# Kernel optimization log

Measured on AMD Instinct MI355X. Metric: run time of the kernel, lower is better.

## Reference

```python
import jax, jax.numpy as jnp
import numpy as np

L, C, S = 4096, 128, 64
SAMPLE_RATE = 4096.0  # Hz; dt offset is 1/sample_rate as in the flax module


def setup_inputs() -> dict:
    key = jax.random.key(0)
    ks = jax.random.split(key, 4)
    x = jax.random.normal(ks[0], (L, C), dtype=jnp.float32)
    # S4D-real init: A = -arange(1, S+1), param stores log(-A) broadcast to (C, S)
    A_log = jnp.broadcast_to(
        jnp.log(jnp.arange(1, S + 1, dtype=jnp.float32)), (C, S)
    )
    sc = 1.0 / np.sqrt(C)  # lecun_normal-like scale for Dense kernels
    B_kernel = (jax.random.normal(ks[1], (C, S)) * sc).astype(jnp.float32)
    B_bias = jnp.zeros((S,), jnp.float32)
    C_kernel = (jax.random.normal(ks[2], (C, S)) * sc).astype(jnp.float32)
    C_bias = jnp.zeros((S,), jnp.float32)
    dt_kernel = (jax.random.normal(ks[3], (C, C)) * sc).astype(jnp.float32)
    dt_bias = jnp.zeros((C,), jnp.float32)
    return {
        "x": x,
        "A_log": A_log,
        "B_kernel": B_kernel,
        "B_bias": B_bias,
        "C_kernel": C_kernel,
        "C_bias": C_bias,
        "dt_kernel": dt_kernel,
        "dt_bias": dt_bias,
    }


def reference(x, A_log, B_kernel, B_bias, C_kernel, C_bias, dt_kernel, dt_bias):
    # ssm params
    A = -jnp.exp(A_log)                                   # (C, S), negative real
    B = 1.0 + x @ B_kernel + B_bias                       # (L, S)
    Cm = x @ C_kernel + C_bias                            # (L, S)
    dt = jax.nn.softplus(1.0 / SAMPLE_RATE + x @ dt_kernel + dt_bias)  # (L, C)
    # discretization (ZOH for diagonal real A)
    At = jnp.exp(A[None, :, :] * dt[:, :, None])          # (L, C, S)
    ut = (At - 1.0) * (B[:, None, :] / A[None, :, :]) * x[:, :, None]  # (L, C, S)

    # parallel linear-recurrence scan: h_t = At_t * h_{t-1} + ut_t, h0 = 0
    def comb(e1, e2):
        a1, u1 = e1
        a2, u2 = e2
        return (a2 * a1, a2 * u1 + u2)

    _, ht = jax.lax.associative_scan(comb, (At, ut))      # scans over axis 0 (L)
    y = jnp.einsum("ls,lcs->lc", Cm, ht)                  # (L, C)
    return y
```

## Files before the change

### kernel.cpp

```cpp
#include <hip/hip_runtime.h>
#include <math.h>

#define LL 4096
#define CC 128
#define SS 64
#define CLEN 32
#define GW 8
#define NG 16
#define CS 8192
#define LOG2E 1.44269504088896f

__global__ __launch_bounds__(256) void k_proj(
    const float* __restrict__ x,
    const float* __restrict__ Bk, const float* __restrict__ Bb,
    const float* __restrict__ Ck, const float* __restrict__ Cb,
    const float* __restrict__ Dk, const float* __restrict__ Db,
    float* __restrict__ Bmat, float* __restrict__ Cmat,
    float* __restrict__ DTmT, float* __restrict__ xT)
{
    __shared__ float xs[CC][20];
    const int r0 = blockIdx.x * 16;
    const int t = threadIdx.x;
    {
        const int r = t >> 4, k8 = (t & 15) * 8;
        const float4 v0 = *(const float4*)&x[(r0 + r) * CC + k8];
        const float4 v1 = *(const float4*)&x[(r0 + r) * CC + k8 + 4];
        xs[k8+0][r] = v0.x; xs[k8+1][r] = v0.y; xs[k8+2][r] = v0.z; xs[k8+3][r] = v0.w;
        xs[k8+4][r] = v1.x; xs[k8+5][r] = v1.y; xs[k8+6][r] = v1.z; xs[k8+7][r] = v1.w;
    }
    __syncthreads();
    {
        const int k = t >> 1, half = (t & 1) * 8;
        const float4 a = *(const float4*)&xs[k][half];
        const float4 b = *(const float4*)&xs[k][half + 4];
        *(float4*)&xT[k * LL + r0 + half]     = a;
        *(float4*)&xT[k * LL + r0 + half + 4] = b;
    }
    const int tc = t & 63, tr = t >> 6;
    const float* Wb; int wstride, wo;
    if (tc < 16)      { Wb = Bk; wstride = SS; wo = 4 * tc; }
    else if (tc < 32) { Wb = Ck; wstride = SS; wo = 4 * tc - 64; }
    else              { Wb = Dk; wstride = CC; wo = 4 * tc - 128; }
    float acc[4][4];
#pragma unroll
    for (int r = 0; r < 4; ++r)
#pragma unroll
        for (int j = 0; j < 4; ++j) acc[r][j] = 0.0f;
    for (int k = 0; k < CC; ++k) {
        const float4 wq = *(const float4*)(Wb + k * wstride + wo);
        const float4 xq = *(const float4*)&xs[k][4 * tr];
        const float wv[4] = {wq.x, wq.y, wq.z, wq.w};
        const float xv[4] = {xq.x, xq.y, xq.z, xq.w};
#pragma unroll
        for (int r = 0; r < 4; ++r)
#pragma unroll
            for (int j = 0; j < 4; ++j) acc[r][j] = fmaf(xv[r], wv[j], acc[r][j]);
    }
    const int rb = r0 + 4 * tr;
    if (tc < 32) {
        const float* bb = (tc < 16) ? Bb : Cb;
        const float add = (tc < 16) ? 1.0f : 0.0f;
        float bias[4];
#pragma unroll
        for (int j = 0; j < 4; ++j) bias[j] = add + bb[wo + j];
        float* dst = (tc < 16) ? Bmat : Cmat;
#pragma unroll
        for (int r = 0; r < 4; ++r) {
            const float4 o = make_float4(acc[r][0] + bias[0], acc[r][1] + bias[1],
                                         acc[r][2] + bias[2], acc[r][3] + bias[3]);
            *(float4*)&dst[(rb + r) * SS + wo] = o;
        }
    } else {
#pragma unroll
        for (int j = 0; j < 4; ++j) {
            const float bj = Db[wo + j] + 0.000244140625f;
            float sp[4];
#pragma unroll
            for (int r = 0; r < 4; ++r) {
                const float z = acc[r][j] + bj;
                sp[r] = fmaxf(z, 0.0f) + log1pf(__expf(-fabsf(z)));
            }
            *(float4*)&DTmT[(wo + j) * LL + rb] = make_float4(sp[0], sp[1], sp[2], sp[3]);
        }
    }
}

__global__ __launch_bounds__(512, 4) void k_sweep1(
    const float* __restrict__ xT, const float* __restrict__ A_log,
    const float* __restrict__ Bmat, const float* __restrict__ DTmT,
    float2* __restrict__ GaGu)
{
    __shared__ float2 agg[GW][SS];
    const int lane = threadIdx.x & 63;
    const int w = __builtin_amdgcn_readfirstlane(threadIdx.x >> 6);
    const int c = blockIdx.x >> 4;
    const int g = blockIdx.x & (NG - 1);
    const int j = c * SS + lane;
    const float A = -__expf(A_log[j]);
    const float A2 = A * LOG2E;
    const float invA = 1.0f / A;
    const int l0 = (g * GW + w) * CLEN;
    const float* dtp = DTmT + c * LL + l0;
    const float* xp  = xT   + c * LL + l0;
    const float* Bp  = Bmat + l0 * SS + lane;
    float ap = 1.0f, uc = 0.0f;
#pragma unroll
    for (int i = 0; i < CLEN; ++i) {
        const float At = __builtin_amdgcn_exp2f(A2 * dtp[i]);
        const float u  = (At - 1.0f) * invA * (Bp[i * SS] * xp[i]);
        ap *= At;
        uc = fmaf(At, uc, u);
    }
    agg[w][lane] = make_float2(ap, uc);
    __syncthreads();
    if (w == 0) {
        float ga = 1.0f, gu = 0.0f;
#pragma unroll
        for (int k = 0; k < GW; ++k) {
            const float2 t = agg[k][lane];
            gu = fmaf(t.x, gu, t.y);
            ga *= t.x;
        }
        GaGu[g * CS + j] = make_float2(ga, gu);
    }
}

__global__ __launch_bounds__(512) void k_emit(
    const float* __restrict__ xT, const float* __restrict__ A_log,
    const float* __restrict__ Bmat, const float* __restrict__ Cmat,
    const float* __restrict__ DTmT,
    const float2* __restrict__ GaGu,
    float* __restrict__ y)
{
    __shared__ float2 agg[GW][SS];
    __shared__ float hgs[SS];
    const int lane = threadIdx.x & 63;
    const int w = __builtin_amdgcn_readfirstlane(threadIdx.x >> 6);
    const int c = blockIdx.x >> 4;
    const int g = blockIdx.x & (NG - 1);
    const int j = c * SS + lane;
    const float A = -__expf(A_log[j]);
    const float A2 = A * LOG2E;
    const float invA = 1.0f / A;
    if (w == 0) {
        float hg = 0.0f;
        float2 ggr[NG - 1];
#pragma unroll
        for (int gg = 0; gg < NG - 1; ++gg) ggr[gg] = GaGu[gg * CS + j];
#pragma unroll
        for (int gg = 0; gg < NG - 1; ++gg)
            hg = (gg < g) ? fmaf(ggr[gg].x, hg, ggr[gg].y) : hg;
        hgs[lane] = hg;
    }
    const int l0 = (g * GW + w) * CLEN;
    const float* dtp = DTmT + c * LL + l0;
    const float* xp  = xT   + c * LL + l0;
    const float* Bp  = Bmat + l0 * SS + lane;
    const float* Cp  = Cmat + l0 * SS + lane;
    float at[CLEN], uu[CLEN];
    {
        float ap = 1.0f, uc = 0.0f;
#pragma unroll
        for (int i = 0; i < CLEN; ++i) {
            at[i] = __builtin_amdgcn_exp2f(A2 * dtp[i]);
            uu[i] = (at[i] - 1.0f) * invA * (Bp[i * SS] * xp[i]);
            ap *= at[i];
            uc = fmaf(at[i], uc, uu[i]);
        }
        agg[w][lane] = make_float2(ap, uc);
    }
    __syncthreads();
    const float hg = hgs[lane];
    float ea = 1.0f, eu = 0.0f;
    for (int k = 0; k < w; ++k) {
        const float2 t = agg[k][lane];
        eu = fmaf(t.x, eu, t.y);
        ea *= t.x;
    }
    float h = fmaf(ea, hg, eu);
#pragma unroll
    for (int i = 0; i < CLEN; ++i) {
        h = fmaf(at[i], h, uu[i]);
        uu[i] = Cp[i * SS] * h;
    }
#pragma unroll
    for (int k = 0; k < 5; ++k) {
        const int d = 1 << k;
        const bool hi = (lane & d) != 0;
#pragma unroll
        for (int i2 = 0; i2 < (CLEN >> (k + 1)); ++i2) {
            const float a = uu[2 * i2], b = uu[2 * i2 + 1];
            const float send = hi ? a : b;
            const float t = __shfl_xor(send, d, 64);
            uu[i2] = (hi ? b : a) + t;
        }
    }
    const float t = __shfl_xor(uu[0], 32, 64);
    const float yv = uu[0] + t;
    if (lane < 32) y[(l0 + lane) * CC + c] = yv;
}

extern "C" void kernel_launch(void* const* d_in, const int* in_sizes, int n_in,
                              void* d_out, int out_size, void* d_ws, size_t ws_size,
                              hipStream_t stream)
{
    const float* x  = (const float*)d_in[0];
    const float* Al = (const float*)d_in[1];
    const float* Bk = (const float*)d_in[2];
    const float* Bb = (const float*)d_in[3];
    const float* Ck = (const float*)d_in[4];
    const float* Cb = (const float*)d_in[5];
    const float* Dk = (const float*)d_in[6];
    const float* Db = (const float*)d_in[7];
    float* y  = (float*)d_out;
    float* ws = (float*)d_ws;

    float*  Bmat = ws;
    float*  Cmat = Bmat + LL * SS;
    float*  DTmT = Cmat + LL * SS;
    float*  xT   = DTmT + CC * LL;
    float2* GaGu = (float2*)(xT + CC * LL);

    k_proj  <<<LL / 16, 256, 0, stream>>>(x, Bk, Bb, Ck, Cb, Dk, Db, Bmat, Cmat, DTmT, xT);
    k_sweep1<<<CC * NG, 512, 0, stream>>>(xT, Al, Bmat, DTmT, GaGu);
    k_emit  <<<CC * NG, 512, 0, stream>>>(xT, Al, Bmat, Cmat, DTmT, GaGu, y);
}
```

Measured before the change: 46.92 us.

## Drop transposed x/dt buffers; stage per-channel dt and x columns in LDS

The projection kernel no longer writes a transposed copy of x, and it stores dt row-major instead of channel-major. The sweep and emit kernels now gather each block's 256 dt and x values for their channel into shared memory with strided loads, then read them from LDS inside the recurrence loop. This removes the transpose writes and their extra global traffic, and replaces the per-lane wave-uniform scalar global loads of dt and x. In exchange, the gather is strided by 128 floats (poorly coalesced), and each block adds an extra barrier before compute.

```diff
diff --git a/kernel.cpp b/kernel.cpp
--- a/kernel.cpp
+++ b/kernel.cpp
@@ -7,6 +7,7 @@
 #define CLEN 32
 #define GW 8
 #define NG 16
+#define GL 256
 #define CS 8192
 #define LOG2E 1.44269504088896f
 
@@ -15,8 +16,7 @@
     const float* __restrict__ Bk, const float* __restrict__ Bb,
     const float* __restrict__ Ck, const float* __restrict__ Cb,
     const float* __restrict__ Dk, const float* __restrict__ Db,
-    float* __restrict__ Bmat, float* __restrict__ Cmat,
-    float* __restrict__ DTmT, float* __restrict__ xT)
+    float* __restrict__ Bmat, float* __restrict__ Cmat, float* __restrict__ DTm)
 {
     __shared__ float xs[CC][20];
     const int r0 = blockIdx.x * 16;
@@ -29,13 +29,6 @@
         xs[k8+4][r] = v1.x; xs[k8+5][r] = v1.y; xs[k8+6][r] = v1.z; xs[k8+7][r] = v1.w;
     }
     __syncthreads();
-    {
-        const int k = t >> 1, half = (t & 1) * 8;
-        const float4 a = *(const float4*)&xs[k][half];
-        const float4 b = *(const float4*)&xs[k][half + 4];
-        *(float4*)&xT[k * LL + r0 + half]     = a;
-        *(float4*)&xT[k * LL + r0 + half + 4] = b;
-    }
     const int tc = t & 63, tr = t >> 6;
     const float* Wb; int wstride, wo;
     if (tc < 16)      { Wb = Bk; wstride = SS; wo = 4 * tc; }
@@ -71,43 +64,50 @@
             *(float4*)&dst[(rb + r) * SS + wo] = o;
         }
     } else {
-#pragma unroll
-        for (int j = 0; j < 4; ++j) {
-            const float bj = Db[wo + j] + 0.000244140625f;
+        float bias[4];
+#pragma unroll
+        for (int j = 0; j < 4; ++j) bias[j] = Db[wo + j] + 0.000244140625f;
+#pragma unroll
+        for (int r = 0; r < 4; ++r) {
             float sp[4];
 #pragma unroll
-            for (int r = 0; r < 4; ++r) {
-                const float z = acc[r][j] + bj;
-                sp[r] = fmaxf(z, 0.0f) + log1pf(__expf(-fabsf(z)));
+            for (int j = 0; j < 4; ++j) {
+                const float z = acc[r][j] + bias[j];
+                sp[j] = fmaxf(z, 0.0f) + log1pf(__expf(-fabsf(z)));
             }
-            *(float4*)&DTmT[(wo + j) * LL + rb] = make_float4(sp[0], sp[1], sp[2], sp[3]);
+            *(float4*)&DTm[(rb + r) * CC + wo] = make_float4(sp[0], sp[1], sp[2], sp[3]);
         }
     }
 }
 
 __global__ __launch_bounds__(512, 4) void k_sweep1(
-    const float* __restrict__ xT, const float* __restrict__ A_log,
-    const float* __restrict__ Bmat, const float* __restrict__ DTmT,
+    const float* __restrict__ x, const float* __restrict__ A_log,
+    const float* __restrict__ Bmat, const float* __restrict__ DTm,
     float2* __restrict__ GaGu)
 {
     __shared__ float2 agg[GW][SS];
-    const int lane = threadIdx.x & 63;
-    const int w = __builtin_amdgcn_readfirstlane(threadIdx.x >> 6);
+    __shared__ float dts[GL];
+    __shared__ float xss[GL];
+    const int t = threadIdx.x;
+    const int lane = t & 63;
+    const int w = __builtin_amdgcn_readfirstlane(t >> 6);
     const int c = blockIdx.x >> 4;
     const int g = blockIdx.x & (NG - 1);
+    const int gl0 = g * GL;
+    if (t < GL) dts[t]      = DTm[(gl0 + t) * CC + c];
+    else        xss[t - GL] = x[(gl0 + (t - GL)) * CC + c];
+    __syncthreads();
     const int j = c * SS + lane;
     const float A = -__expf(A_log[j]);
     const float A2 = A * LOG2E;
     const float invA = 1.0f / A;
-    const int l0 = (g * GW + w) * CLEN;
-    const float* dtp = DTmT + c * LL + l0;
-    const float* xp  = xT   + c * LL + l0;
-    const float* Bp  = Bmat + l0 * SS + lane;
+    const int lw = w * CLEN;
+    const float* Bp = Bmat + (gl0 + lw) * SS + lane;
     float ap = 1.0f, uc = 0.0f;
 #pragma unroll
     for (int i = 0; i < CLEN; ++i) {
-        const float At = __builtin_amdgcn_exp2f(A2 * dtp[i]);
-        const float u  = (At - 1.0f) * invA * (Bp[i * SS] * xp[i]);
+        const float At = __builtin_amdgcn_exp2f(A2 * dts[lw + i]);
+        const float u  = (At - 1.0f) * invA * (Bp[i * SS] * xss[lw + i]);
         ap *= At;
         uc = fmaf(At, uc, u);
     }
@@ -117,27 +117,33 @@
         float ga = 1.0f, gu = 0.0f;
 #pragma unroll
         for (int k = 0; k < GW; ++k) {
-            const float2 t = agg[k][lane];
-            gu = fmaf(t.x, gu, t.y);
-            ga *= t.x;
+            const float2 tt = agg[k][lane];
+            gu = fmaf(tt.x, gu, tt.y);
+            ga *= tt.x;
         }
         GaGu[g * CS + j] = make_float2(ga, gu);
     }
 }
 
 __global__ __launch_bounds__(512) void k_emit(
-    const float* __restrict__ xT, const float* __restrict__ A_log,
+    const float* __restrict__ x, const float* __restrict__ A_log,
     const float* __restrict__ Bmat, const float* __restrict__ Cmat,
-    const float* __restrict__ DTmT,
+    const float* __restrict__ DTm,
     const float2* __restrict__ GaGu,
     float* __restrict__ y)
 {
     __shared__ float2 agg[GW][SS];
     __shared__ float hgs[SS];
-    const int lane = threadIdx.x & 63;
-    const int w = __builtin_amdgcn_readfirstlane(threadIdx.x >> 6);
+    __shared__ float dts[GL];
+    __shared__ float xss[GL];
+    const int t = threadIdx.x;
+    const int lane = t & 63;
+    const int w = __builtin_amdgcn_readfirstlane(t >> 6);
     const int c = blockIdx.x >> 4;
     const int g = blockIdx.x & (NG - 1);
+    const int gl0 = g * GL;
+    if (t < GL) dts[t]      = DTm[(gl0 + t) * CC + c];
+    else        xss[t - GL] = x[(gl0 + (t - GL)) * CC + c];
     const int j = c * SS + lane;
     const float A = -__expf(A_log[j]);
     const float A2 = A * LOG2E;
@@ -152,18 +158,17 @@
             hg = (gg < g) ? fmaf(ggr[gg].x, hg, ggr[gg].y) : hg;
         hgs[lane] = hg;
     }
-    const int l0 = (g * GW + w) * CLEN;
-    const float* dtp = DTmT + c * LL + l0;
-    const float* xp  = xT   + c * LL + l0;
-    const float* Bp  = Bmat + l0 * SS + lane;
-    const float* Cp  = Cmat + l0 * SS + lane;
+    __syncthreads();
+    const int lw = w * CLEN;
+    const float* Bp = Bmat + (gl0 + lw) * SS + lane;
+    const float* Cp = Cmat + (gl0 + lw) * SS + lane;
     float at[CLEN], uu[CLEN];
     {
         float ap = 1.0f, uc = 0.0f;
 #pragma unroll
         for (int i = 0; i < CLEN; ++i) {
-            at[i] = __builtin_amdgcn_exp2f(A2 * dtp[i]);
-            uu[i] = (at[i] - 1.0f) * invA * (Bp[i * SS] * xp[i]);
+            at[i] = __builtin_amdgcn_exp2f(A2 * dts[lw + i]);
+            uu[i] = (at[i] - 1.0f) * invA * (Bp[i * SS] * xss[lw + i]);
             ap *= at[i];
             uc = fmaf(at[i], uc, uu[i]);
         }
@@ -173,9 +178,9 @@
     const float hg = hgs[lane];
     float ea = 1.0f, eu = 0.0f;
     for (int k = 0; k < w; ++k) {
-        const float2 t = agg[k][lane];
-        eu = fmaf(t.x, eu, t.y);
-        ea *= t.x;
+        const float2 tt = agg[k][lane];
+        eu = fmaf(tt.x, eu, tt.y);
+        ea *= tt.x;
     }
     float h = fmaf(ea, hg, eu);
 #pragma unroll
@@ -191,13 +196,13 @@
         for (int i2 = 0; i2 < (CLEN >> (k + 1)); ++i2) {
             const float a = uu[2 * i2], b = uu[2 * i2 + 1];
             const float send = hi ? a : b;
-            const float t = __shfl_xor(send, d, 64);
-            uu[i2] = (hi ? b : a) + t;
-        }
-    }
-    const float t = __shfl_xor(uu[0], 32, 64);
-    const float yv = uu[0] + t;
-    if (lane < 32) y[(l0 + lane) * CC + c] = yv;
+            const float tt = __shfl_xor(send, d, 64);
+            uu[i2] = (hi ? b : a) + tt;
+        }
+    }
+    const float tt = __shfl_xor(uu[0], 32, 64);
+    const float yv = uu[0] + tt;
+    if (lane < 32) y[(gl0 + lw + lane) * CC + c] = yv;
 }
 
 extern "C" void kernel_launch(void* const* d_in, const int* in_sizes, int n_in,
@@ -217,11 +222,10 @@
 
     float*  Bmat = ws;
     float*  Cmat = Bmat + LL * SS;
-    float*  DTmT = Cmat + LL * SS;
-    float*  xT   = DTmT + CC * LL;
-    float2* GaGu = (float2*)(xT + CC * LL);
-
-    k_proj  <<<LL / 16, 256, 0, stream>>>(x, Bk, Bb, Ck, Cb, Dk, Db, Bmat, Cmat, DTmT, xT);
-    k_sweep1<<<CC * NG, 512, 0, stream>>>(xT, Al, Bmat, DTmT, GaGu);
-    k_emit  <<<CC * NG, 512, 0, stream>>>(xT, Al, Bmat, Cmat, DTmT, GaGu, y);
-}
+    float*  DTm  = Cmat + LL * SS;
+    float2* GaGu = (float2*)(DTm + LL * CC);
+
+    k_proj  <<<LL / 16, 256, 0, stream>>>(x, Bk, Bb, Ck, Cb, Dk, Db, Bmat, Cmat, DTm);
+    k_sweep1<<<CC * NG, 512, 0, stream>>>(x, Al, Bmat, DTm, GaGu);
+    k_emit  <<<CC * NG, 512, 0, stream>>>(x, Al, Bmat, Cmat, DTm, GaGu, y);
+}
```

Measured after the change: 52.93 us. 1.13x slower.
